# Kernel tuning notes

Measured on AMD Instinct MI355X. Metric: run time of the kernel, lower is better.

The kernel has to match this reference:

```python
import jax, jax.numpy as jnp
import numpy as np

EMB = 1024
HID = 1536
NE = 8


def setup_inputs() -> dict:
    key = jax.random.key(0)
    ks = jax.random.split(key, 8)
    B, N, E, H, ne = 4, 2048, EMB, HID, NE
    s = 1.0 / np.sqrt(E)
    sh = 1.0 / np.sqrt(H)
    return {
        "x": jax.random.normal(ks[0], (B, N, E), dtype=jnp.float32),
        "Wr": jax.random.uniform(ks[1], (E, ne), minval=-s, maxval=s, dtype=jnp.float32),
        "br": jax.random.uniform(ks[2], (ne,), minval=-s, maxval=s, dtype=jnp.float32),
        "W1": jax.random.uniform(ks[3], (ne, E, H), minval=-s, maxval=s, dtype=jnp.float32),
        "b1": jax.random.uniform(ks[4], (ne, H), minval=-s, maxval=s, dtype=jnp.float32),
        "W2": jax.random.uniform(ks[5], (ne, H, E), minval=-sh, maxval=sh, dtype=jnp.float32),
        "b2": jax.random.uniform(ks[6], (ne, E), minval=-sh, maxval=sh, dtype=jnp.float32),
        "k": 2,
    }


def reference(x, Wr, br, W1, b1, W2, b2, k):
    B, N, E = x.shape
    T = B * N
    ne = Wr.shape[1]
    flat = x.reshape(T, E)
    logits = flat @ Wr + br                      # [T, ne]
    _, topk_idx = jax.lax.top_k(logits, k)       # [T, k]
    # counts[t, e] = number of top-k slots of token t assigned to expert e
    counts = jax.nn.one_hot(topk_idx, ne, dtype=flat.dtype).sum(axis=1)  # [T, ne]
    out = jnp.zeros_like(flat)
    for e in range(ne):  # small fixed loop over experts (structurally distinct weights)
        h = jax.nn.gelu(flat @ W1[e] + b1[e], approximate=False)  # torch nn.GELU = exact erf
        y = h @ W2[e] + b2[e]
        out = out + counts[:, e:e + 1] * y
    out = out / k
    return out.reshape(B, N, E)
```

## Files before the change

kernel.cpp:

```cpp
#include <hip/hip_runtime.h>
#include <hip/hip_bf16.h>
#include <math.h>

#define T_TOK 8192
#define EMB   1024
#define HID   1536
#define NE    8
#define NBINB 64
#define BINTOK (T_TOK / NBINB)

typedef float  floatx4 __attribute__((ext_vector_type(4)));
typedef __bf16 bf16x8  __attribute__((ext_vector_type(8)));

#define WS_COUNTS   0
#define WS_OFFSETS  1024
#define WS_FLAGS    2048
#define WS_BHIST    4096
#define WS_TOKMAP   8192
#define WS_TOKLIST  270336
#define WS_YBUF     532480
#define WS_W1T      34086912
#define WS_W2T      59252736
#define WS_H        84418560
#define WS_NEEDED   135143424

__device__ __forceinline__ float eload(const void* p, size_t idx, bool f32) {
  return f32 ? ((const float*)p)[idx] : (float)(((const __bf16*)p)[idx]);
}

__device__ __forceinline__ bf16x8 ld8f32(const void* p, size_t idx) {
  const float* g = (const float*)p + idx;
  float4 u = *(const float4*)g;
  float4 v = *(const float4*)(g + 4);
  bf16x8 r;
  r[0] = (__bf16)u.x; r[1] = (__bf16)u.y; r[2] = (__bf16)u.z; r[3] = (__bf16)u.w;
  r[4] = (__bf16)v.x; r[5] = (__bf16)v.y; r[6] = (__bf16)v.z; r[7] = (__bf16)v.w;
  return r;
}

__device__ __forceinline__ void glds16(const void* g, void* l) {
  __builtin_amdgcn_global_load_lds(
      (const __attribute__((address_space(1))) unsigned int*)g,
      (__attribute__((address_space(3))) unsigned int*)l, 16, 0, 0);
}

__global__ __launch_bounds__(256)
void sniff_kernel(const void* p0, const void* p1, const void* p2, const void* p3,
                  const void* p4, const void* p5, const void* p6, int* flags) {
  const void* ps[7] = {p0, p1, p2, p3, p4, p5, p6};
  const int nelem[7] = {T_TOK * EMB, EMB * NE, NE, NE * EMB * HID, NE * HID, NE * HID * EMB, NE * EMB};
  int t = blockIdx.x;
  const unsigned* w = (const unsigned*)ps[t];
  int nw = nelem[t] / 2;
  if (nw > 2048) nw = 2048;
  __shared__ int s_pl, s_nz;
  if (threadIdx.x == 0) { s_pl = 0; s_nz = 0; }
  __syncthreads();
  int pl = 0, nz = 0;
  for (int i = threadIdx.x; i < nw; i += 256) {
    unsigned v = w[i];
    if (v == 0) continue;
    nz++;
    unsigned e = (v >> 23) & 0xFF;
    if (e >= 100 && e <= 150) pl++;
  }
  atomicAdd(&s_pl, pl);
  atomicAdd(&s_nz, nz);
  __syncthreads();
  if (threadIdx.x == 0) flags[t] = (2 * s_pl > s_nz) ? 1 : 0;
}

__global__ __launch_bounds__(256)
void logits_kernel(const void* __restrict__ x, const void* __restrict__ Wr,
                   const void* __restrict__ br, const int* __restrict__ kptr,
                   const int* __restrict__ flags, int* __restrict__ topk) {
  const bool xf32  = flags[0] != 0;
  const bool wrf32 = flags[1] != 0;
  const bool brf32 = flags[2] != 0;
  const int wave = threadIdx.x >> 6;
  const int lane = threadIdx.x & 63;
  const int t = blockIdx.x * 4 + wave;

  float xv[16];
  {
    size_t base = (size_t)t * EMB + lane * 16;
    if (xf32) {
      const float* g = (const float*)x + base;
#pragma unroll
      for (int j = 0; j < 16; ++j) xv[j] = g[j];
    } else {
      bf16x8 u = *(const bf16x8*)((const __bf16*)x + base);
      bf16x8 v = *(const bf16x8*)((const __bf16*)x + base + 8);
#pragma unroll
      for (int j = 0; j < 8; ++j) { xv[j] = (float)u[j]; xv[8 + j] = (float)v[j]; }
    }
  }
  float acc[NE];
#pragma unroll
  for (int e = 0; e < NE; ++e) acc[e] = 0.f;
  if (wrf32) {
#pragma unroll
    for (int j = 0; j < 16; ++j) {
      const float* wr = (const float*)Wr + (size_t)(lane * 16 + j) * NE;
#pragma unroll
      for (int e = 0; e < NE; ++e) acc[e] += xv[j] * wr[e];
    }
  } else {
#pragma unroll
    for (int j = 0; j < 16; ++j) {
      bf16x8 wr = *(const bf16x8*)((const __bf16*)Wr + (size_t)(lane * 16 + j) * NE);
#pragma unroll
      for (int e = 0; e < NE; ++e) acc[e] += xv[j] * (float)wr[e];
    }
  }
#pragma unroll
  for (int e = 0; e < NE; ++e) {
#pragma unroll
    for (int off = 32; off > 0; off >>= 1)
      acc[e] += __shfl_xor(acc[e], off, 64);
  }
  if (lane == 0) {
    int k = kptr[0];
    if (k < 1) k = 1; if (k > NE) k = NE;
    float lg[NE];
#pragma unroll
    for (int e = 0; e < NE; ++e) lg[e] = acc[e] + eload(br, e, brf32);
    for (int s = 0; s < k; ++s) {
      int bi = 0; float bv = lg[0];
#pragma unroll
      for (int e = 1; e < NE; ++e) { if (lg[e] > bv) { bv = lg[e]; bi = e; } }
      lg[bi] = -3.0e38f;
      topk[t * 8 + s] = bi;
    }
  }
}

__global__ __launch_bounds__(128)
void bin1_kernel(const int* __restrict__ topk, const int* __restrict__ kptr,
                 int* __restrict__ bhist) {
  __shared__ int lhist[NE];
  if (threadIdx.x < NE) lhist[threadIdx.x] = 0;
  __syncthreads();
  int k = kptr[0];
  if (k < 1) k = 1; if (k > NE) k = NE;
  const int t = blockIdx.x * BINTOK + threadIdx.x;
  for (int s = 0; s < k; ++s) atomicAdd(&lhist[topk[t * 8 + s] & 7], 1);
  __syncthreads();
  if (threadIdx.x < NE) bhist[blockIdx.x * NE + threadIdx.x] = lhist[threadIdx.x];
}

__global__ __launch_bounds__(256)
void scan_kernel(int* __restrict__ bhist, int* __restrict__ counts, int* __restrict__ offsets) {
  __shared__ int sh[NBINB * NE];
  __shared__ int scnt[NE];
  __shared__ int soff[NE + 1];
  const int tid = threadIdx.x;
  for (int i = tid; i < NBINB * NE; i += 256) sh[i] = bhist[i];
  __syncthreads();
  if (tid < NE) {
    int s = 0;
    for (int b = 0; b < NBINB; ++b) s += sh[b * NE + tid];
    scnt[tid] = s;
  }
  __syncthreads();
  if (tid == 0) {
    int s = 0;
    for (int e = 0; e < NE; ++e) { soff[e] = s; s += scnt[e]; }
    soff[NE] = s;
  }
  __syncthreads();
  if (tid < NE) {
    int run = soff[tid];
    for (int b = 0; b < NBINB; ++b) {
      int v = sh[b * NE + tid];
      sh[b * NE + tid] = run;
      run += v;
    }
  }
  __syncthreads();
  for (int i = tid; i < NBINB * NE; i += 256) bhist[i] = sh[i];
  if (tid < NE) counts[tid] = scnt[tid];
  if (tid < NE + 1) offsets[tid] = soff[tid];
}

__global__ __launch_bounds__(128)
void bin2_kernel(const int* __restrict__ bhist, const int* __restrict__ offsets,
                 const int* __restrict__ kptr,
                 int* __restrict__ tok_list, int* __restrict__ tokmap) {
  __shared__ int lbase[NE];
  __shared__ int lcnt[NE];
  if (threadIdx.x < NE) {
    lbase[threadIdx.x] = bhist[blockIdx.x * NE + threadIdx.x];
    lcnt[threadIdx.x] = 0;
  }
  __syncthreads();
  int k = kptr[0];
  if (k < 1) k = 1; if (k > NE) k = NE;
  const int t = blockIdx.x * BINTOK + threadIdx.x;
  for (int s = 0; s < k; ++s) {
    int e = tokmap[t * 8 + s] & 7;
    int pos = atomicAdd(&lcnt[e], 1);
    int grow = lbase[e] + pos;
    tok_list[e * T_TOK + (grow - offsets[e])] = t;
    tokmap[t * 8 + s] = (e << 16) | grow;
  }
}

__global__ __launch_bounds__(256)
void transpose_kernel(const void* __restrict__ in, __bf16* __restrict__ out, int K, int N,
                      const int* __restrict__ flags, int fidx) {
  const bool f32 = flags[fidx] != 0;
  __shared__ __bf16 tile[64][65];
  size_t eoff = (size_t)blockIdx.z * (size_t)K * (size_t)N;
  int n0 = blockIdx.x * 64;
  int k0 = blockIdx.y * 64;
  int tx = threadIdx.x & 63;
  int ty = threadIdx.x >> 6;
#pragma unroll
  for (int i = 0; i < 16; ++i) {
    int r = i * 4 + ty;
    tile[r][tx] = (__bf16)eload(in, eoff + (size_t)(k0 + r) * N + (n0 + tx), f32);
  }
  __syncthreads();
#pragma unroll
  for (int i = 0; i < 16; ++i) {
    int r = i * 4 + ty;
    out[eoff + (size_t)(n0 + r) * K + (k0 + tx)] = tile[tx][r];
  }
}

__global__ __launch_bounds__(256, 2)
void gemm1_kernel(const void* __restrict__ x, const __bf16* __restrict__ w1t,
                  const void* __restrict__ b1, const int* __restrict__ counts,
                  const int* __restrict__ offsets, const int* __restrict__ tok_list,
                  const int* __restrict__ flags, __bf16* __restrict__ hbuf) {
  const int flat = blockIdx.x;
  const int e   = flat & 7;
  const int idx = flat >> 3;
  const int mTg = idx / 96;
  const int sub = idx % 96;
  const int nT  = sub >> 3;
  const int mT  = mTg * 8 + (sub & 7);
  const int cnt = counts[e];
  if (mT * 128 >= cnt) return;
  const bool xf32  = flags[0] != 0;
  const bool b1f32 = flags[4] != 0;

  __shared__ __align__(16) __bf16 As[128 * 32];
  __shared__ __align__(16) __bf16 Bs[128 * 32];

  const int wave = threadIdx.x >> 6;
  const int lane = threadIdx.x & 63;
  const int sr = lane >> 2;
  const int kc = (lane & 3) * 8;
  const int r0 = wave * 16 + sr;
  const int r1 = 64 + wave * 16 + sr;

  const int tokA0 = tok_list[e * T_TOK + mT * 128 + r0];
  const int tokA1 = tok_list[e * T_TOK + mT * 128 + r1];
  const __bf16* xb = (const __bf16*)x;
  const __bf16* gA0 = xb + (size_t)tokA0 * EMB + kc;
  const __bf16* gA1 = xb + (size_t)tokA1 * EMB + kc;
  const __bf16* gB0 = w1t + ((size_t)e * HID + nT * 128 + r0) * EMB + kc;
  const __bf16* gB1 = w1t + ((size_t)e * HID + nT * 128 + r1) * EMB + kc;

  __bf16* lA0 = As + (wave * 16) * 32;
  __bf16* lA1 = As + (64 + wave * 16) * 32;
  __bf16* lB0 = Bs + (wave * 16) * 32;
  __bf16* lB1 = Bs + (64 + wave * 16) * 32;

  const int wm = (wave & 1) * 64;
  const int wn = (wave >> 1) * 64;
  const int mr = lane & 15;
  const int kq8 = (lane >> 4) * 8;

  floatx4 acc[4][4];
#pragma unroll
  for (int i = 0; i < 4; ++i)
#pragma unroll
    for (int j = 0; j < 4; ++j) acc[i][j] = (floatx4){0.f, 0.f, 0.f, 0.f};

  if (!xf32) {
    for (int kb = 0; kb < EMB / 32; ++kb) {
      __syncthreads();
      glds16(gA0, lA0); glds16(gA1, lA1);
      glds16(gB0, lB0); glds16(gB1, lB1);
      gA0 += 32; gA1 += 32; gB0 += 32; gB1 += 32;
      __syncthreads();
      bf16x8 af[4], bfr[4];
#pragma unroll
      for (int i = 0; i < 4; ++i) af[i]  = *(const bf16x8*)(As + (wm + i * 16 + mr) * 32 + kq8);
#pragma unroll
      for (int j = 0; j < 4; ++j) bfr[j] = *(const bf16x8*)(Bs + (wn + j * 16 + mr) * 32 + kq8);
#pragma unroll
      for (int i = 0; i < 4; ++i)
#pragma unroll
        for (int j = 0; j < 4; ++j)
          acc[i][j] = __builtin_amdgcn_mfma_f32_16x16x32_bf16(af[i], bfr[j], acc[i][j], 0, 0, 0);
    }
  } else {
    size_t oA0 = (size_t)tokA0 * EMB + kc, oA1 = (size_t)tokA1 * EMB + kc;
    for (int kb = 0; kb < EMB / 32; ++kb) {
      bf16x8 a0 = ld8f32(x, oA0 + kb * 32);
      bf16x8 a1 = ld8f32(x, oA1 + kb * 32);
      bf16x8 b0 = *(const bf16x8*)(gB0 + kb * 32);
      bf16x8 b1v = *(const bf16x8*)(gB1 + kb * 32);
      __syncthreads();
      *(bf16x8*)(As + r0 * 32 + kc) = a0;
      *(bf16x8*)(As + r1 * 32 + kc) = a1;
      *(bf16x8*)(Bs + r0 * 32 + kc) = b0;
      *(bf16x8*)(Bs + r1 * 32 + kc) = b1v;
      __syncthreads();
      bf16x8 af[4], bfr[4];
#pragma unroll
      for (int i = 0; i < 4; ++i) af[i]  = *(const bf16x8*)(As + (wm + i * 16 + mr) * 32 + kq8);
#pragma unroll
      for (int j = 0; j < 4; ++j) bfr[j] = *(const bf16x8*)(Bs + (wn + j * 16 + mr) * 32 + kq8);
#pragma unroll
      for (int i = 0; i < 4; ++i)
#pragma unroll
        for (int j = 0; j < 4; ++j)
          acc[i][j] = __builtin_amdgcn_mfma_f32_16x16x32_bf16(af[i], bfr[j], acc[i][j], 0, 0, 0);
    }
  }

  const int hBase   = offsets[e] + mT * 128;
  const int colBase = nT * 128 + wn + mr;
  float b1v4[4];
#pragma unroll
  for (int j = 0; j < 4; ++j) b1v4[j] = eload(b1, (size_t)e * HID + colBase + j * 16, b1f32);
#pragma unroll
  for (int i = 0; i < 4; ++i) {
    const int rowLoc = wm + i * 16 + (lane >> 4) * 4;
#pragma unroll
    for (int r = 0; r < 4; ++r) {
      const int row = rowLoc + r;
      if (mT * 128 + row < cnt) {
        __bf16* hp = hbuf + (size_t)(hBase + row) * HID + colBase;
#pragma unroll
        for (int j = 0; j < 4; ++j) {
          float v = acc[i][j][r] + b1v4[j];
          float g = 0.5f * v * (1.0f + erff(v * 0.70710678118654752f));
          hp[j * 16] = (__bf16)g;
        }
      }
    }
  }
}

__global__ __launch_bounds__(256, 2)
void gemm2_kernel(const __bf16* __restrict__ hbuf, const __bf16* __restrict__ w2t,
                  const void* __restrict__ b2, const int* __restrict__ counts,
                  const int* __restrict__ offsets, const int* __restrict__ flags,
                  __bf16* __restrict__ ybuf) {
  const int flat = blockIdx.x;
  const int e   = flat & 7;
  const int idx = flat >> 3;
  const int mTg = idx >> 6;
  const int sub = idx & 63;
  const int nT  = sub >> 3;
  const int mT  = mTg * 8 + (sub & 7);
  const int cnt = counts[e];
  if (mT * 128 >= cnt) return;
  const bool b2f32 = flags[6] != 0;

  __shared__ __align__(16) __bf16 As[128 * 32];
  __shared__ __align__(16) __bf16 Bs[128 * 32];

  const int wave = threadIdx.x >> 6;
  const int lane = threadIdx.x & 63;
  const int sr = lane >> 2;
  const int kc = (lane & 3) * 8;
  const int r0 = wave * 16 + sr;
  const int r1 = 64 + wave * 16 + sr;

  const int rowBase = offsets[e] + mT * 128;
  const __bf16* gA0 = hbuf + (size_t)(rowBase + r0) * HID + kc;
  const __bf16* gA1 = hbuf + (size_t)(rowBase + r1) * HID + kc;
  const __bf16* gB0 = w2t + ((size_t)e * EMB + nT * 128 + r0) * HID + kc;
  const __bf16* gB1 = w2t + ((size_t)e * EMB + nT * 128 + r1) * HID + kc;

  const int wm = (wave & 1) * 64;
  const int wn = (wave >> 1) * 64;
  const int mr = lane & 15;
  const int kq8 = (lane >> 4) * 8;

  floatx4 acc[4][4];
#pragma unroll
  for (int i = 0; i < 4; ++i)
#pragma unroll
    for (int j = 0; j < 4; ++j) acc[i][j] = (floatx4){0.f, 0.f, 0.f, 0.f};

  bf16x8 s0 = *(const bf16x8*)gA0, s1 = *(const bf16x8*)gA1;
  bf16x8 s2 = *(const bf16x8*)gB0, s3 = *(const bf16x8*)gB1;
  const int niter = HID / 32;
  for (int kb = 0; kb < niter; ++kb) {
    bf16x8 n0 = s0, n1 = s1, n2 = s2, n3 = s3;
    if (kb + 1 < niter) {
      gA0 += 32; gA1 += 32; gB0 += 32; gB1 += 32;
      n0 = *(const bf16x8*)gA0; n1 = *(const bf16x8*)gA1;
      n2 = *(const bf16x8*)gB0; n3 = *(const bf16x8*)gB1;
    }
    __syncthreads();
    *(bf16x8*)(As + r0 * 32 + kc) = s0;
    *(bf16x8*)(As + r1 * 32 + kc) = s1;
    *(bf16x8*)(Bs + r0 * 32 + kc) = s2;
    *(bf16x8*)(Bs + r1 * 32 + kc) = s3;
    __syncthreads();
    bf16x8 af[4], bfr[4];
#pragma unroll
    for (int i = 0; i < 4; ++i) af[i]  = *(const bf16x8*)(As + (wm + i * 16 + mr) * 32 + kq8);
#pragma unroll
    for (int j = 0; j < 4; ++j) bfr[j] = *(const bf16x8*)(Bs + (wn + j * 16 + mr) * 32 + kq8);
#pragma unroll
    for (int i = 0; i < 4; ++i)
#pragma unroll
      for (int j = 0; j < 4; ++j)
        acc[i][j] = __builtin_amdgcn_mfma_f32_16x16x32_bf16(af[i], bfr[j], acc[i][j], 0, 0, 0);
    s0 = n0; s1 = n1; s2 = n2; s3 = n3;
  }

  const int colBase = nT * 128 + wn + mr;
  float b2v4[4];
#pragma unroll
  for (int j = 0; j < 4; ++j) b2v4[j] = eload(b2, (size_t)e * EMB + colBase + j * 16, b2f32);
#pragma unroll
  for (int i = 0; i < 4; ++i) {
    const int rowLoc = wm + i * 16 + (lane >> 4) * 4;
#pragma unroll
    for (int r = 0; r < 4; ++r) {
      const int row = rowLoc + r;
      if (mT * 128 + row < cnt) {
        __bf16* yp = ybuf + (size_t)(rowBase + row) * EMB + colBase;
#pragma unroll
        for (int j = 0; j < 4; ++j)
          yp[j * 16] = (__bf16)(acc[i][j][r] + b2v4[j]);
      }
    }
  }
}

__global__ __launch_bounds__(256)
void combine_kernel(const __bf16* __restrict__ ybuf, const int* __restrict__ tokmap,
                    const int* __restrict__ kptr, const int* __restrict__ flags,
                    void* __restrict__ out) {
  const bool f32 = flags[0] != 0;
  const int wave = threadIdx.x >> 6;
  const int lane = threadIdx.x & 63;
  const int t = blockIdx.x * 4 + wave;
  int k = kptr[0];
  if (k < 1) k = 1; if (k > NE) k = NE;
  const float invk = 1.0f / (float)k;
  int rows[NE];
  for (int s = 0; s < k; ++s) rows[s] = tokmap[t * 8 + s] & 0xFFFF;
#pragma unroll
  for (int c = 0; c < 2; ++c) {
    const int i = c * 512 + lane * 8;
    float a[8];
#pragma unroll
    for (int j = 0; j < 8; ++j) a[j] = 0.f;
    for (int s = 0; s < k; ++s) {
      bf16x8 y = *(const bf16x8*)(ybuf + (size_t)rows[s] * EMB + i);
#pragma unroll
      for (int j = 0; j < 8; ++j) a[j] += (float)y[j];
    }
    if (f32) {
      float* op = (float*)out + (size_t)t * EMB + i;
      float4 u = {a[0] * invk, a[1] * invk, a[2] * invk, a[3] * invk};
      float4 v = {a[4] * invk, a[5] * invk, a[6] * invk, a[7] * invk};
      *(float4*)op = u;
      *(float4*)(op + 4) = v;
    } else {
      bf16x8 o;
#pragma unroll
      for (int j = 0; j < 8; ++j) o[j] = (__bf16)(a[j] * invk);
      *(bf16x8*)((__bf16*)out + (size_t)t * EMB + i) = o;
    }
  }
}

extern "C" void kernel_launch(void* const* d_in, const int* in_sizes, int n_in,
                              void* d_out, int out_size, void* d_ws, size_t ws_size,
                              hipStream_t stream) {
  (void)in_sizes; (void)n_in; (void)out_size;
  if (ws_size < (size_t)WS_NEEDED) return;

  const void* x  = d_in[0];
  const void* Wr = d_in[1];
  const void* br = d_in[2];
  const void* W1 = d_in[3];
  const void* b1 = d_in[4];
  const void* W2 = d_in[5];
  const void* b2 = d_in[6];
  const int* kptr = (const int*)d_in[7];

  char* ws = (char*)d_ws;
  int*    counts   = (int*)(ws + WS_COUNTS);
  int*    offsets  = (int*)(ws + WS_OFFSETS);
  int*    flags    = (int*)(ws + WS_FLAGS);
  int*    bhist    = (int*)(ws + WS_BHIST);
  int*    tokmap   = (int*)(ws + WS_TOKMAP);
  int*    tok_list = (int*)(ws + WS_TOKLIST);
  __bf16* ybuf     = (__bf16*)(ws + WS_YBUF);
  __bf16* w1t      = (__bf16*)(ws + WS_W1T);
  __bf16* w2t      = (__bf16*)(ws + WS_W2T);
  __bf16* hbuf     = (__bf16*)(ws + WS_H);

  hipMemsetAsync(ws, 0, WS_YBUF, stream);

  sniff_kernel<<<dim3(7), 256, 0, stream>>>(x, Wr, br, W1, b1, W2, b2, flags);

  transpose_kernel<<<dim3(HID / 64, EMB / 64, NE), 256, 0, stream>>>(W1, w1t, EMB, HID, flags, 3);
  transpose_kernel<<<dim3(EMB / 64, HID / 64, NE), 256, 0, stream>>>(W2, w2t, HID, EMB, flags, 5);

  logits_kernel<<<dim3(T_TOK / 4), 256, 0, stream>>>(x, Wr, br, kptr, flags, tokmap);
  bin1_kernel<<<dim3(NBINB), 128, 0, stream>>>(tokmap, kptr, bhist);
  scan_kernel<<<dim3(1), 256, 0, stream>>>(bhist, counts, offsets);
  bin2_kernel<<<dim3(NBINB), 128, 0, stream>>>(bhist, offsets, kptr, tok_list, tokmap);

  gemm1_kernel<<<dim3(8 * 64 * (HID / 128)), 256, 0, stream>>>(
      x, w1t, b1, counts, offsets, tok_list, flags, hbuf);
  gemm2_kernel<<<dim3(8 * 64 * (EMB / 128)), 256, 0, stream>>>(
      hbuf, w2t, b2, counts, offsets, flags, ybuf);

  combine_kernel<<<dim3(T_TOK / 4), 256, 0, stream>>>(ybuf, tokmap, kptr, flags, d_out);
}
```

Baseline: 439.8 us.

## Use 256x256 tiles with 4-stage async LDS pipeline and pre-converted bf16 x

The logits kernel now also writes a bf16 copy of x, so gemm1 always takes the direct global-to-LDS path and the fp32 conversion branch is gone. Both expert GEMMs move to 512-thread blocks with 256x256 output tiles. Each uses a 4-slot LDS ring with loads issued three k-steps ahead, waits via vmcnt, XOR-swizzled LDS layout, and raised MFMA priority. This aims to hide global latency, remove per-step double syncthreads, and improve data reuse, at the cost of large LDS use (128KB) and more tile-tail waste on small experts. The bf16 x copy reuses the ybuf region, which gemm2 later overwrites.

```diff
diff --git a/kernel.cpp b/kernel.cpp
--- a/kernel.cpp
+++ b/kernel.cpp
@@ -28,16 +28,6 @@
   return f32 ? ((const float*)p)[idx] : (float)(((const __bf16*)p)[idx]);
 }
 
-__device__ __forceinline__ bf16x8 ld8f32(const void* p, size_t idx) {
-  const float* g = (const float*)p + idx;
-  float4 u = *(const float4*)g;
-  float4 v = *(const float4*)(g + 4);
-  bf16x8 r;
-  r[0] = (__bf16)u.x; r[1] = (__bf16)u.y; r[2] = (__bf16)u.z; r[3] = (__bf16)u.w;
-  r[4] = (__bf16)v.x; r[5] = (__bf16)v.y; r[6] = (__bf16)v.z; r[7] = (__bf16)v.w;
-  return r;
-}
-
 __device__ __forceinline__ void glds16(const void* g, void* l) {
   __builtin_amdgcn_global_load_lds(
       (const __attribute__((address_space(1))) unsigned int*)g,
@@ -73,7 +63,8 @@
 __global__ __launch_bounds__(256)
 void logits_kernel(const void* __restrict__ x, const void* __restrict__ Wr,
                    const void* __restrict__ br, const int* __restrict__ kptr,
-                   const int* __restrict__ flags, int* __restrict__ topk) {
+                   const int* __restrict__ flags, int* __restrict__ topk,
+                   __bf16* __restrict__ xbf) {
   const bool xf32  = flags[0] != 0;
   const bool wrf32 = flags[1] != 0;
   const bool brf32 = flags[2] != 0;
@@ -94,6 +85,14 @@
 #pragma unroll
       for (int j = 0; j < 8; ++j) { xv[j] = (float)u[j]; xv[8 + j] = (float)v[j]; }
     }
+  }
+  {
+    bf16x8 o0, o1;
+#pragma unroll
+    for (int j = 0; j < 8; ++j) { o0[j] = (__bf16)xv[j]; o1[j] = (__bf16)xv[8 + j]; }
+    __bf16* xo = xbf + (size_t)t * EMB + lane * 16;
+    *(bf16x8*)xo = o0;
+    *(bf16x8*)(xo + 8) = o1;
   }
   float acc[NE];
 #pragma unroll
@@ -229,117 +228,108 @@
   }
 }
 
-__global__ __launch_bounds__(256, 2)
-void gemm1_kernel(const void* __restrict__ x, const __bf16* __restrict__ w1t,
+
+#define STAGE4(TT) do {                                                  \
+    const int _sl = (TT) & 3;                                            \
+    __bf16* _dA = ldsA + _sl * 8192 + wave * 512;                        \
+    __bf16* _dB = ldsB + _sl * 8192 + wave * 512;                        \
+    const size_t _ko = (size_t)(TT) * 32;                                \
+    glds16(pA0 + _ko, _dA);                                              \
+    glds16(pA1 + _ko, _dA + 4096);                                       \
+    glds16(pB0 + _ko, _dB);                                              \
+    glds16(pB1 + _ko, _dB + 4096);                                       \
+  } while (0)
+
+#define KSTEP(TT, WAITS, DOSTAGE) do {                                   \
+    asm volatile(WAITS ::: "memory");                                    \
+    __builtin_amdgcn_s_barrier();                                        \
+    const char* _aS = (const char*)(ldsA + ((TT) & 3) * 8192);           \
+    const char* _bS = (const char*)(ldsB + ((TT) & 3) * 8192);           \
+    bf16x8 _af[8], _bf[4];                                               \
+    _Pragma("unroll")                                                    \
+    for (int _i = 0; _i < 8; ++_i) _af[_i] = *(const bf16x8*)(_aS + aOff[_i]); \
+    _Pragma("unroll")                                                    \
+    for (int _j = 0; _j < 4; ++_j) _bf[_j] = *(const bf16x8*)(_bS + bOff[_j]); \
+    if (DOSTAGE) STAGE4((TT) + 3);                                       \
+    __builtin_amdgcn_s_setprio(1);                                       \
+    _Pragma("unroll")                                                    \
+    for (int _i = 0; _i < 8; ++_i)                                       \
+      _Pragma("unroll")                                                  \
+      for (int _j = 0; _j < 4; ++_j)                                     \
+        acc[_i][_j] = __builtin_amdgcn_mfma_f32_16x16x32_bf16(_af[_i], _bf[_j], acc[_i][_j], 0, 0, 0); \
+    __builtin_amdgcn_s_setprio(0);                                       \
+  } while (0)
+
+__global__ __launch_bounds__(512, 2)
+void gemm1_kernel(const __bf16* __restrict__ xbf, const __bf16* __restrict__ w1t,
                   const void* __restrict__ b1, const int* __restrict__ counts,
                   const int* __restrict__ offsets, const int* __restrict__ tok_list,
                   const int* __restrict__ flags, __bf16* __restrict__ hbuf) {
   const int flat = blockIdx.x;
   const int e   = flat & 7;
   const int idx = flat >> 3;
-  const int mTg = idx / 96;
-  const int sub = idx % 96;
-  const int nT  = sub >> 3;
-  const int mT  = mTg * 8 + (sub & 7);
+  const int mT  = idx / 6;
+  const int nT  = idx % 6;
   const int cnt = counts[e];
-  if (mT * 128 >= cnt) return;
-  const bool xf32  = flags[0] != 0;
+  if (mT * 256 >= cnt) return;
   const bool b1f32 = flags[4] != 0;
 
-  __shared__ __align__(16) __bf16 As[128 * 32];
-  __shared__ __align__(16) __bf16 Bs[128 * 32];
-
-  const int wave = threadIdx.x >> 6;
-  const int lane = threadIdx.x & 63;
-  const int sr = lane >> 2;
-  const int kc = (lane & 3) * 8;
-  const int r0 = wave * 16 + sr;
-  const int r1 = 64 + wave * 16 + sr;
-
-  const int tokA0 = tok_list[e * T_TOK + mT * 128 + r0];
-  const int tokA1 = tok_list[e * T_TOK + mT * 128 + r1];
-  const __bf16* xb = (const __bf16*)x;
-  const __bf16* gA0 = xb + (size_t)tokA0 * EMB + kc;
-  const __bf16* gA1 = xb + (size_t)tokA1 * EMB + kc;
-  const __bf16* gB0 = w1t + ((size_t)e * HID + nT * 128 + r0) * EMB + kc;
-  const __bf16* gB1 = w1t + ((size_t)e * HID + nT * 128 + r1) * EMB + kc;
-
-  __bf16* lA0 = As + (wave * 16) * 32;
-  __bf16* lA1 = As + (64 + wave * 16) * 32;
-  __bf16* lB0 = Bs + (wave * 16) * 32;
-  __bf16* lB1 = Bs + (64 + wave * 16) * 32;
-
-  const int wm = (wave & 1) * 64;
-  const int wn = (wave >> 1) * 64;
-  const int mr = lane & 15;
-  const int kq8 = (lane >> 4) * 8;
-
-  floatx4 acc[4][4];
-#pragma unroll
-  for (int i = 0; i < 4; ++i)
+  __shared__ __align__(16) __bf16 ldsA[4 * 8192];
+  __shared__ __align__(16) __bf16 ldsB[4 * 8192];
+
+  const int tid  = threadIdx.x;
+  const int wave = tid >> 6;
+  const int lane = tid & 63;
+
+  const int sr = wave * 16 + (lane >> 2);
+  const int cA = lane & 3;
+  const int cg = cA ^ ((sr >> 1) & 3);
+  const int tokA0 = tok_list[e * T_TOK + mT * 256 + sr];
+  const int tokA1 = tok_list[e * T_TOK + mT * 256 + 128 + sr];
+  const __bf16* pA0 = xbf + (size_t)tokA0 * EMB + cg * 8;
+  const __bf16* pA1 = xbf + (size_t)tokA1 * EMB + cg * 8;
+  const __bf16* pB0 = w1t + ((size_t)e * HID + nT * 256 + sr) * EMB + cg * 8;
+  const __bf16* pB1 = w1t + ((size_t)e * HID + nT * 256 + 128 + sr) * EMB + cg * 8;
+
+  const int wm = (wave >> 2) * 128;
+  const int wn = (wave & 3) * 64;
+  const int fr = lane & 15;
+  const int fc = lane >> 4;
+  int aOff[8], bOff[4];
+#pragma unroll
+  for (int i = 0; i < 8; ++i) { int R = wm + i * 16 + fr; aOff[i] = R * 64 + ((fc ^ ((R >> 1) & 3)) << 4); }
+#pragma unroll
+  for (int j = 0; j < 4; ++j) { int R = wn + j * 16 + fr; bOff[j] = R * 64 + ((fc ^ ((R >> 1) & 3)) << 4); }
+
+  floatx4 acc[8][4];
+#pragma unroll
+  for (int i = 0; i < 8; ++i)
 #pragma unroll
     for (int j = 0; j < 4; ++j) acc[i][j] = (floatx4){0.f, 0.f, 0.f, 0.f};
 
-  if (!xf32) {
-    for (int kb = 0; kb < EMB / 32; ++kb) {
-      __syncthreads();
-      glds16(gA0, lA0); glds16(gA1, lA1);
-      glds16(gB0, lB0); glds16(gB1, lB1);
-      gA0 += 32; gA1 += 32; gB0 += 32; gB1 += 32;
-      __syncthreads();
-      bf16x8 af[4], bfr[4];
-#pragma unroll
-      for (int i = 0; i < 4; ++i) af[i]  = *(const bf16x8*)(As + (wm + i * 16 + mr) * 32 + kq8);
-#pragma unroll
-      for (int j = 0; j < 4; ++j) bfr[j] = *(const bf16x8*)(Bs + (wn + j * 16 + mr) * 32 + kq8);
-#pragma unroll
-      for (int i = 0; i < 4; ++i)
-#pragma unroll
-        for (int j = 0; j < 4; ++j)
-          acc[i][j] = __builtin_amdgcn_mfma_f32_16x16x32_bf16(af[i], bfr[j], acc[i][j], 0, 0, 0);
-    }
-  } else {
-    size_t oA0 = (size_t)tokA0 * EMB + kc, oA1 = (size_t)tokA1 * EMB + kc;
-    for (int kb = 0; kb < EMB / 32; ++kb) {
-      bf16x8 a0 = ld8f32(x, oA0 + kb * 32);
-      bf16x8 a1 = ld8f32(x, oA1 + kb * 32);
-      bf16x8 b0 = *(const bf16x8*)(gB0 + kb * 32);
-      bf16x8 b1v = *(const bf16x8*)(gB1 + kb * 32);
-      __syncthreads();
-      *(bf16x8*)(As + r0 * 32 + kc) = a0;
-      *(bf16x8*)(As + r1 * 32 + kc) = a1;
-      *(bf16x8*)(Bs + r0 * 32 + kc) = b0;
-      *(bf16x8*)(Bs + r1 * 32 + kc) = b1v;
-      __syncthreads();
-      bf16x8 af[4], bfr[4];
-#pragma unroll
-      for (int i = 0; i < 4; ++i) af[i]  = *(const bf16x8*)(As + (wm + i * 16 + mr) * 32 + kq8);
-#pragma unroll
-      for (int j = 0; j < 4; ++j) bfr[j] = *(const bf16x8*)(Bs + (wn + j * 16 + mr) * 32 + kq8);
-#pragma unroll
-      for (int i = 0; i < 4; ++i)
-#pragma unroll
-        for (int j = 0; j < 4; ++j)
-          acc[i][j] = __builtin_amdgcn_mfma_f32_16x16x32_bf16(af[i], bfr[j], acc[i][j], 0, 0, 0);
-    }
-  }
-
-  const int hBase   = offsets[e] + mT * 128;
-  const int colBase = nT * 128 + wn + mr;
-  float b1v4[4];
-#pragma unroll
-  for (int j = 0; j < 4; ++j) b1v4[j] = eload(b1, (size_t)e * HID + colBase + j * 16, b1f32);
-#pragma unroll
-  for (int i = 0; i < 4; ++i) {
-    const int rowLoc = wm + i * 16 + (lane >> 4) * 4;
+  STAGE4(0); STAGE4(1); STAGE4(2);
+  const int nk = EMB / 32;
+#pragma unroll 2
+  for (int t = 0; t < nk - 2; ++t) KSTEP(t, "s_waitcnt vmcnt(8)", (t + 3 < nk));
+  KSTEP(nk - 2, "s_waitcnt vmcnt(4)", 0);
+  KSTEP(nk - 1, "s_waitcnt vmcnt(0)", 0);
+
+  const int hBase   = offsets[e] + mT * 256;
+  const int colBase = nT * 256 + wn + fr;
+  float bv[4];
+#pragma unroll
+  for (int j = 0; j < 4; ++j) bv[j] = eload(b1, (size_t)e * HID + colBase + j * 16, b1f32);
+#pragma unroll
+  for (int i = 0; i < 8; ++i) {
+    const int rowLoc = wm + i * 16 + fc * 4;
 #pragma unroll
     for (int r = 0; r < 4; ++r) {
       const int row = rowLoc + r;
-      if (mT * 128 + row < cnt) {
+      if (mT * 256 + row < cnt) {
         __bf16* hp = hbuf + (size_t)(hBase + row) * HID + colBase;
 #pragma unroll
         for (int j = 0; j < 4; ++j) {
-          float v = acc[i][j][r] + b1v4[j];
+          float v = acc[i][j][r] + bv[j];
           float g = 0.5f * v * (1.0f + erff(v * 0.70710678118654752f));
           hp[j * 16] = (__bf16)g;
         }
@@ -348,7 +338,7 @@
   }
 }
 
-__global__ __launch_bounds__(256, 2)
+__global__ __launch_bounds__(512, 2)
 void gemm2_kernel(const __bf16* __restrict__ hbuf, const __bf16* __restrict__ w2t,
                   const void* __restrict__ b2, const int* __restrict__ counts,
                   const int* __restrict__ offsets, const int* __restrict__ flags,
@@ -356,85 +346,69 @@
   const int flat = blockIdx.x;
   const int e   = flat & 7;
   const int idx = flat >> 3;
-  const int mTg = idx >> 6;
-  const int sub = idx & 63;
-  const int nT  = sub >> 3;
-  const int mT  = mTg * 8 + (sub & 7);
+  const int mT  = idx >> 2;
+  const int nT  = idx & 3;
   const int cnt = counts[e];
-  if (mT * 128 >= cnt) return;
+  if (mT * 256 >= cnt) return;
   const bool b2f32 = flags[6] != 0;
 
-  __shared__ __align__(16) __bf16 As[128 * 32];
-  __shared__ __align__(16) __bf16 Bs[128 * 32];
-
-  const int wave = threadIdx.x >> 6;
-  const int lane = threadIdx.x & 63;
-  const int sr = lane >> 2;
-  const int kc = (lane & 3) * 8;
-  const int r0 = wave * 16 + sr;
-  const int r1 = 64 + wave * 16 + sr;
-
-  const int rowBase = offsets[e] + mT * 128;
-  const __bf16* gA0 = hbuf + (size_t)(rowBase + r0) * HID + kc;
-  const __bf16* gA1 = hbuf + (size_t)(rowBase + r1) * HID + kc;
-  const __bf16* gB0 = w2t + ((size_t)e * EMB + nT * 128 + r0) * HID + kc;
-  const __bf16* gB1 = w2t + ((size_t)e * EMB + nT * 128 + r1) * HID + kc;
-
-  const int wm = (wave & 1) * 64;
-  const int wn = (wave >> 1) * 64;
-  const int mr = lane & 15;
-  const int kq8 = (lane >> 4) * 8;
-
-  floatx4 acc[4][4];
-#pragma unroll
-  for (int i = 0; i < 4; ++i)
+  __shared__ __align__(16) __bf16 ldsA[4 * 8192];
+  __shared__ __align__(16) __bf16 ldsB[4 * 8192];
+
+  const int tid  = threadIdx.x;
+  const int wave = tid >> 6;
+  const int lane = tid & 63;
+
+  const int sr = wave * 16 + (lane >> 2);
+  const int cA = lane & 3;
+  const int cg = cA ^ ((sr >> 1) & 3);
+  const int rowBase = offsets[e] + mT * 256;
+  const int lastRow = offsets[NE] - 1;
+  const int rA0 = min(rowBase + sr, lastRow);
+  const int rA1 = min(rowBase + 128 + sr, lastRow);
+  const __bf16* pA0 = hbuf + (size_t)rA0 * HID + cg * 8;
+  const __bf16* pA1 = hbuf + (size_t)rA1 * HID + cg * 8;
+  const __bf16* pB0 = w2t + ((size_t)e * EMB + nT * 256 + sr) * HID + cg * 8;
+  const __bf16* pB1 = w2t + ((size_t)e * EMB + nT * 256 + 128 + sr) * HID + cg * 8;
+
+  const int wm = (wave >> 2) * 128;
+  const int wn = (wave & 3) * 64;
+  const int fr = lane & 15;
+  const int fc = lane >> 4;
+  int aOff[8], bOff[4];
+#pragma unroll
+  for (int i = 0; i < 8; ++i) { int R = wm + i * 16 + fr; aOff[i] = R * 64 + ((fc ^ ((R >> 1) & 3)) << 4); }
+#pragma unroll
+  for (int j = 0; j < 4; ++j) { int R = wn + j * 16 + fr; bOff[j] = R * 64 + ((fc ^ ((R >> 1) & 3)) << 4); }
+
+  floatx4 acc[8][4];
+#pragma unroll
+  for (int i = 0; i < 8; ++i)
 #pragma unroll
     for (int j = 0; j < 4; ++j) acc[i][j] = (floatx4){0.f, 0.f, 0.f, 0.f};
 
-  bf16x8 s0 = *(const bf16x8*)gA0, s1 = *(const bf16x8*)gA1;
-  bf16x8 s2 = *(const bf16x8*)gB0, s3 = *(const bf16x8*)gB1;
-  const int niter = HID / 32;
-  for (int kb = 0; kb < niter; ++kb) {
-    bf16x8 n0 = s0, n1 = s1, n2 = s2, n3 = s3;
-    if (kb + 1 < niter) {
-      gA0 += 32; gA1 += 32; gB0 += 32; gB1 += 32;
-      n0 = *(const bf16x8*)gA0; n1 = *(const bf16x8*)gA1;
-      n2 = *(const bf16x8*)gB0; n3 = *(const bf16x8*)gB1;
-    }
-    __syncthreads();
-    *(bf16x8*)(As + r0 * 32 + kc) = s0;
-    *(bf16x8*)(As + r1 * 32 + kc) = s1;
-    *(bf16x8*)(Bs + r0 * 32 + kc) = s2;
-    *(bf16x8*)(Bs + r1 * 32 + kc) = s3;
-    __syncthreads();
-    bf16x8 af[4], bfr[4];
-#pragma unroll
-    for (int i = 0; i < 4; ++i) af[i]  = *(const bf16x8*)(As + (wm + i * 16 + mr) * 32 + kq8);
-#pragma unroll
-    for (int j = 0; j < 4; ++j) bfr[j] = *(const bf16x8*)(Bs + (wn + j * 16 + mr) * 32 + kq8);
-#pragma unroll
-    for (int i = 0; i < 4; ++i)
-#pragma unroll
-      for (int j = 0; j < 4; ++j)
-        acc[i][j] = __builtin_amdgcn_mfma_f32_16x16x32_bf16(af[i], bfr[j], acc[i][j], 0, 0, 0);
-    s0 = n0; s1 = n1; s2 = n2; s3 = n3;
-  }
-
-  const int colBase = nT * 128 + wn + mr;
-  float b2v4[4];
-#pragma unroll
-  for (int j = 0; j < 4; ++j) b2v4[j] = eload(b2, (size_t)e * EMB + colBase + j * 16, b2f32);
-#pragma unroll
-  for (int i = 0; i < 4; ++i) {
-    const int rowLoc = wm + i * 16 + (lane >> 4) * 4;
+  STAGE4(0); STAGE4(1); STAGE4(2);
+  const int nk = HID / 32;
+#pragma unroll 2
+  for (int t = 0; t < nk - 2; ++t) KSTEP(t, "s_waitcnt vmcnt(8)", (t + 3 < nk));
+  KSTEP(nk - 2, "s_waitcnt vmcnt(4)", 0);
+  KSTEP(nk - 1, "s_waitcnt vmcnt(0)", 0);
+
+  const int colBase = nT * 256 + wn + fr;
+  float bv[4];
+#pragma unroll
+  for (int j = 0; j < 4; ++j) bv[j] = eload(b2, (size_t)e * EMB + colBase + j * 16, b2f32);
+#pragma unroll
+  for (int i = 0; i < 8; ++i) {
+    const int rowLoc = wm + i * 16 + fc * 4;
 #pragma unroll
     for (int r = 0; r < 4; ++r) {
       const int row = rowLoc + r;
-      if (mT * 128 + row < cnt) {
+      if (mT * 256 + row < cnt) {
         __bf16* yp = ybuf + (size_t)(rowBase + row) * EMB + colBase;
 #pragma unroll
         for (int j = 0; j < 4; ++j)
-          yp[j * 16] = (__bf16)(acc[i][j][r] + b2v4[j]);
+          yp[j * 16] = (__bf16)(acc[i][j][r] + bv[j]);
       }
     }
   }
@@ -502,6 +476,7 @@
   int*    tokmap   = (int*)(ws + WS_TOKMAP);
   int*    tok_list = (int*)(ws + WS_TOKLIST);
   __bf16* ybuf     = (__bf16*)(ws + WS_YBUF);
+  __bf16* xbf      = (__bf16*)(ws + WS_YBUF);
   __bf16* w1t      = (__bf16*)(ws + WS_W1T);
   __bf16* w2t      = (__bf16*)(ws + WS_W2T);
   __bf16* hbuf     = (__bf16*)(ws + WS_H);
@@ -513,14 +488,14 @@
   transpose_kernel<<<dim3(HID / 64, EMB / 64, NE), 256, 0, stream>>>(W1, w1t, EMB, HID, flags, 3);
   transpose_kernel<<<dim3(EMB / 64, HID / 64, NE), 256, 0, stream>>>(W2, w2t, HID, EMB, flags, 5);
 
-  logits_kernel<<<dim3(T_TOK / 4), 256, 0, stream>>>(x, Wr, br, kptr, flags, tokmap);
+  logits_kernel<<<dim3(T_TOK / 4), 256, 0, stream>>>(x, Wr, br, kptr, flags, tokmap, xbf);
   bin1_kernel<<<dim3(NBINB), 128, 0, stream>>>(tokmap, kptr, bhist);
   scan_kernel<<<dim3(1), 256, 0, stream>>>(bhist, counts, offsets);
   bin2_kernel<<<dim3(NBINB), 128, 0, stream>>>(bhist, offsets, kptr, tok_list, tokmap);
 
-  gemm1_kernel<<<dim3(8 * 64 * (HID / 128)), 256, 0, stream>>>(
-      x, w1t, b1, counts, offsets, tok_list, flags, hbuf);
-  gemm2_kernel<<<dim3(8 * 64 * (EMB / 128)), 256, 0, stream>>>(
+  gemm1_kernel<<<dim3(8 * 32 * 6), 512, 0, stream>>>(
+      xbf, w1t, b1, counts, offsets, tok_list, flags, hbuf);
+  gemm2_kernel<<<dim3(8 * 32 * 4), 512, 0, stream>>>(
       hbuf, w2t, b2, counts, offsets, flags, ybuf);
 
   combine_kernel<<<dim3(T_TOK / 4), 256, 0, stream>>>(ybuf, tokmap, kptr, flags, d_out);
```

After: 424.8 us. 3.4% less time.
